# Kernel optimization log

Hardware: AMD Instinct MI355X
Metric: run time of the kernel (lower is better)

The kernel has to match this reference:

```python
import jax, jax.numpy as jnp
import numpy as np

EPS = 1e-6

def setup_inputs() -> dict:
    key = jax.random.key(0)
    ks = jax.random.split(key, 8)
    I, S, O = 1024, 512, 1024
    Bsz, T = 4, 2048
    return {
        "u": jax.random.normal(ks[0], (Bsz, T, I), dtype=jnp.float32),
        "dt": jax.random.normal(ks[1], (S,), dtype=jnp.float32),
        "A": jax.random.normal(ks[2], (S,), dtype=jnp.float32),
        "Bmat": jax.random.normal(ks[3], (I, S), dtype=jnp.float32) / np.sqrt(S),
        "C": jax.random.normal(ks[4], (S, O), dtype=jnp.float32) / np.sqrt(S),
        "D": jax.random.normal(ks[5], (O,), dtype=jnp.float32),
        "norm_w": jnp.ones((I,), dtype=jnp.float32),
    }

def _rmsnorm(x, w):
    x32 = x.astype(jnp.float32)
    n = x32 * jax.lax.rsqrt(jnp.mean(x32 * x32, axis=-1, keepdims=True) + EPS)
    return n.astype(x.dtype) * w

def reference(u, dt, A, Bmat, C, D, norm_w):
    u = _rmsnorm(u, norm_w)                      # [B, T, I]
    Bsz, T, _ = u.shape
    dts = jax.nn.sigmoid(dt)                     # [S]
    a = jnp.exp(-dts * jnp.abs(A))               # [S] discretized decay
    t = jnp.arange(T, dtype=jnp.float32)
    h = dts[:, None] * a[:, None] ** t[None, :]  # [S, T] geometric kernel
    u_proj = jnp.einsum('bti,is->bst', u, Bmat)  # [B, S, T]
    # depthwise causal conv: flipped kernel + cross-correlation == convolution
    k = jnp.flip(h, axis=1)[:, None, :]          # [S, 1, T] (OIW)
    x = jax.lax.conv_general_dilated(
        u_proj, k, window_strides=(1,), padding=[(T - 1, T - 1)],
        dimension_numbers=('NCW', 'OIW', 'NCW'),
        feature_group_count=u_proj.shape[1])[:, :, :T]  # [B, S, T]
    x = jnp.transpose(x, (0, 2, 1))              # [B, T, S]
    y = jnp.einsum('bts,so->bto', x, C) + D      # [B, T, O]
    return (y, x[:, -1])
```

## Files before the change

### kernel.cpp

```cpp
#include <hip/hip_runtime.h>
#include <math.h>

#define I_DIM 1024
#define S_DIM 512
#define O_DIM 1024
#define T_DIM 2048
#define B_SZ 4
#define M_ROWS (B_SZ * T_DIM)
#define EPSF 1e-6f

#define CL 64
#define NCH 32

typedef _Float16 f16;
typedef __attribute__((ext_vector_type(8))) _Float16 f16x8;
typedef __attribute__((ext_vector_type(2))) _Float16 f16x2;
typedef __attribute__((ext_vector_type(4))) float f32x4;

__device__ __forceinline__ unsigned short f2h_bits(float f) {
    _Float16 h = (_Float16)f;
    return __builtin_bit_cast(unsigned short, h);
}

__device__ __forceinline__ void load16_lds(const void* g, void* l) {
    __builtin_amdgcn_global_load_lds((const __attribute__((address_space(1))) void*)g,
                                     (__attribute__((address_space(3))) void*)l,
                                     16, 0, 0);
}

__global__ __launch_bounds__(256)
void prep(const float* __restrict__ u, const float* __restrict__ nw,
          unsigned short* __restrict__ u16,
          const float* __restrict__ Bmat, const float* __restrict__ dt,
          unsigned short* __restrict__ Bt16,
          const float* __restrict__ Cmat, unsigned short* __restrict__ Ct16) {
    __shared__ float tile[32][33];
    const int t = threadIdx.x;
    const int bx = blockIdx.x;

    if (bx < M_ROWS) {
        float4 v = ((const float4*)(u + (size_t)bx * I_DIM))[t];
        float ss = v.x * v.x + v.y * v.y + v.z * v.z + v.w * v.w;
        #pragma unroll
        for (int off = 32; off > 0; off >>= 1) ss += __shfl_down(ss, off, 64);
        if ((t & 63) == 0) tile[0][t >> 6] = ss;
        __syncthreads();
        if (t == 0)
            tile[0][0] = rsqrtf((tile[0][0] + tile[0][1] + tile[0][2] + tile[0][3])
                                * (1.0f / I_DIM) + EPSF);
        __syncthreads();
        const float rs = tile[0][0];
        ushort4 o;
        o.x = f2h_bits(v.x * rs);
        o.y = f2h_bits(v.y * rs);
        o.z = f2h_bits(v.z * rs);
        o.w = f2h_bits(v.w * rs);
        ((ushort4*)(u16 + (size_t)bx * I_DIM))[t] = o;
    } else if (bx < M_ROWS + 512) {
        const int tb = bx - M_ROWS;
        const int bs = (tb & 15) * 32;
        const int bi = (tb >> 4) * 32;
        const int tx = t & 31, ty = t >> 5;
        #pragma unroll
        for (int i = ty; i < 32; i += 8)
            tile[i][tx] = Bmat[(size_t)(bi + i) * S_DIM + bs + tx];
        __syncthreads();
        const float w = nw[bi + tx];
        #pragma unroll
        for (int i = ty; i < 32; i += 8) {
            const int s = bs + i;
            const float dts = 1.0f / (1.0f + expf(-dt[s]));
            Bt16[(size_t)s * I_DIM + bi + tx] = f2h_bits(tile[tx][i] * dts * w);
        }
    } else {
        const int tb = bx - M_ROWS - 512;
        const int bo = (tb & 31) * 32;
        const int bs = (tb >> 5) * 32;
        const int tx = t & 31, ty = t >> 5;
        #pragma unroll
        for (int i = ty; i < 32; i += 8)
            tile[i][tx] = Cmat[(size_t)(bs + i) * O_DIM + bo + tx];
        __syncthreads();
        #pragma unroll
        for (int i = ty; i < 32; i += 8)
            Ct16[(size_t)(bo + i) * S_DIM + bs + tx] = f2h_bits(tile[tx][i]);
    }
}

__global__ __launch_bounds__(256)
void gemm1_chfin(const f16* __restrict__ A, const f16* __restrict__ Bt,
                 f16* __restrict__ up, float* __restrict__ chlast,
                 const float* __restrict__ dt, const float* __restrict__ Avec) {
    constexpr int K = I_DIM, N = S_DIM, NK = K / 32;
    __shared__ f16 As[3][64 * 32];
    __shared__ f16 Bs[3][128 * 32];
    const int t = threadIdx.x;

    int bid = blockIdx.x;
    bid = (bid & 7) * 64 + (bid >> 3);
    const int n0 = (bid & 3) * 128;
    const int m0 = (bid >> 2) * 64;
    const int wid = t >> 6, lane = t & 63;
    const int wn = wid * 32, lr = lane & 15, kg = lane >> 4;

    const int srcswz = ((t & 3) ^ ((t >> 3) & 3)) * 8;
    const f16* aptr = A + (size_t)(m0 + (t >> 2)) * K + srcswz;
    const f16* bptr = Bt + (size_t)(n0 + (t >> 2)) * K + srcswz;
    const int rchunk = (kg ^ ((lr >> 1) & 3)) * 8;

    f32x4 acc[4][2];
    #pragma unroll
    for (int i = 0; i < 4; ++i)
        #pragma unroll
        for (int j = 0; j < 2; ++j) acc[i][j] = (f32x4){0.f, 0.f, 0.f, 0.f};

    auto stage = [&](int kt, int buf) {
        const int k0 = kt * 32;
        load16_lds(aptr + k0, &As[buf][t * 8]);
        load16_lds(bptr + k0, &Bs[buf][t * 8]);
        load16_lds(bptr + (size_t)64 * K + k0, &Bs[buf][2048 + t * 8]);
    };

    stage(0, 0);
    stage(1, 1);
    int bcur = 0, bst = 2;
    for (int kt = 0; kt < NK; ++kt) {
        if (kt + 1 < NK) asm volatile("s_waitcnt vmcnt(3)");
        else             asm volatile("s_waitcnt vmcnt(0)");
        __builtin_amdgcn_s_barrier();
        __builtin_amdgcn_sched_barrier(0);
        if (kt + 2 < NK) stage(kt + 2, bst);

        f16x8 af[4], bf[2];
        #pragma unroll
        for (int m = 0; m < 4; ++m)
            af[m] = *(const f16x8*)&As[bcur][(m * 16 + lr) * 32 + rchunk];
        #pragma unroll
        for (int n = 0; n < 2; ++n)
            bf[n] = *(const f16x8*)&Bs[bcur][(wn + n * 16 + lr) * 32 + rchunk];
        #pragma unroll
        for (int m = 0; m < 4; ++m)
            #pragma unroll
            for (int n = 0; n < 2; ++n)
                acc[m][n] = __builtin_amdgcn_mfma_f32_16x16x32_f16(af[m], bf[n], acc[m][n], 0, 0, 0);

        bcur = (bcur == 2) ? 0 : bcur + 1;
        bst  = (bst  == 2) ? 0 : bst  + 1;
    }

    const int cb = m0 >> 11;
    const int cc = (m0 >> 6) & (NCH - 1);
    #pragma unroll
    for (int n = 0; n < 2; ++n) {
        const int col = n0 + wn + n * 16 + lr;
        const float dts = 1.0f / (1.0f + expf(-dt[col]));
        const float e = dts * fabsf(Avec[col]);
        const float ainv = expf(e);
        float partial = 0.f;
        #pragma unroll
        for (int m = 0; m < 4; ++m) {
            const int row = m * 16 + kg * 4;
            float wgt = expf(-e * (float)(63 - row));
            #pragma unroll
            for (int j = 0; j < 4; ++j) {
                const float val = acc[m][n][j];
                up[(size_t)(m0 + row + j) * N + col] = (_Float16)val;
                partial = fmaf(wgt, val, partial);
                wgt *= ainv;
            }
        }
        partial += __shfl_xor(partial, 16, 64);
        partial += __shfl_xor(partial, 32, 64);
        if (kg == 0)
            chlast[(size_t)(cb * NCH + cc) * S_DIM + col] = partial;
    }
}

__global__ __launch_bounds__(256)
void gemm2_scan(const f16* __restrict__ upb, const float* __restrict__ chlast,
                const f16* __restrict__ Ct, const float* __restrict__ Dvec,
                const float* __restrict__ dt, const float* __restrict__ Avec,
                float* __restrict__ y, float* __restrict__ xlast) {
    constexpr int K = S_DIM, N = O_DIM, NK = K / 32;
    __shared__ __align__(16) unsigned char As[64 * 1024];
    __shared__ f16 Bs[2][128 * 32];
    const int t = threadIdx.x;

    int bid = blockIdx.x;
    bid = (bid & 7) * 128 + (bid >> 3);
    const int n0 = (bid & 7) * 128;
    const int m0 = (bid >> 3) * 64;
    const int wid = t >> 6, lane = t & 63;
    const int wn = wid * 32, lr = lane & 15, kg = lane >> 4;

    const int srcswz = ((t & 3) ^ ((t >> 3) & 3)) * 8;
    const f16* bptr = Ct + (size_t)(n0 + (t >> 2)) * K + srcswz;
    load16_lds(bptr, &Bs[0][t * 8]);
    load16_lds(bptr + (size_t)64 * K, &Bs[0][2048 + t * 8]);
    const int rchunk = (kg ^ ((lr >> 1) & 3)) * 8;

    const int cc = (m0 >> 6) & (NCH - 1);
    const int cb = m0 >> 11;
    const int s0 = 2 * t;
    const float dts0 = 1.0f / (1.0f + expf(-dt[s0]));
    const float dts1 = 1.0f / (1.0f + expf(-dt[s0 + 1]));
    const float ab0 = fabsf(Avec[s0]), ab1 = fabsf(Avec[s0 + 1]);
    const float g0 = expf(-dts0 * ab0);
    const float g1 = expf(-dts1 * ab1);
    const float gCL0 = expf(-dts0 * ab0 * (float)CL);
    const float gCL1 = expf(-dts1 * ab1 * (float)CL);
    const float2* ch = (const float2*)chlast;
    float cy0 = 0.f, cy1 = 0.f;
    {
        int j = 0;
        for (; j + 4 <= cc; j += 4) {
            float2 f0 = ch[(size_t)(cb * NCH + j + 0) * 256 + t];
            float2 f1 = ch[(size_t)(cb * NCH + j + 1) * 256 + t];
            float2 f2 = ch[(size_t)(cb * NCH + j + 2) * 256 + t];
            float2 f3 = ch[(size_t)(cb * NCH + j + 3) * 256 + t];
            cy0 = fmaf(gCL0, cy0, f0.x); cy1 = fmaf(gCL1, cy1, f0.y);
            cy0 = fmaf(gCL0, cy0, f1.x); cy1 = fmaf(gCL1, cy1, f1.y);
            cy0 = fmaf(gCL0, cy0, f2.x); cy1 = fmaf(gCL1, cy1, f2.y);
            cy0 = fmaf(gCL0, cy0, f3.x); cy1 = fmaf(gCL1, cy1, f3.y);
        }
        for (; j < cc; ++j) {
            float2 f = ch[(size_t)(cb * NCH + j) * 256 + t];
            cy0 = fmaf(gCL0, cy0, f.x);
            cy1 = fmaf(gCL1, cy1, f.y);
        }
    }

    const unsigned* up32 = (const unsigned*)upb;
    const size_t ub = (size_t)m0 * 256 + t;
    unsigned v[CL];
    #pragma unroll
    for (int j = 0; j < CL; ++j) v[j] = up32[ub + (size_t)j * 256];
    float x0 = cy0, x1 = cy1;
    #pragma unroll
    for (int j = 0; j < CL; ++j) {
        f16x2 h = __builtin_bit_cast(f16x2, v[j]);
        x0 = fmaf(g0, x0, (float)h.x);
        x1 = fmaf(g1, x1, (float)h.y);
        f16x2 o; o.x = (_Float16)x0; o.y = (_Float16)x1;
        v[j] = __builtin_bit_cast(unsigned, o);
    }
    #pragma unroll
    for (int j = 0; j < CL; ++j)
        *(unsigned*)&As[j * 1024 + ((t * 4) ^ ((j & 7) << 4))] = v[j];
    if (cc == NCH - 1)
        ((float2*)xlast)[cb * 256 + t] = make_float2(x0, x1);
    __syncthreads();

    f32x4 acc[4][2];
    #pragma unroll
    for (int i = 0; i < 4; ++i)
        #pragma unroll
        for (int j = 0; j < 2; ++j) acc[i][j] = (f32x4){0.f, 0.f, 0.f, 0.f};

    const int swz = (lr & 7) << 4;
    for (int kt = 0; kt < NK; ++kt) {
        const int cur = kt & 1;
        if (kt + 1 < NK) {
            const int k1 = (kt + 1) * 32;
            load16_lds(bptr + k1, &Bs[cur ^ 1][t * 8]);
            load16_lds(bptr + (size_t)64 * K + k1, &Bs[cur ^ 1][2048 + t * 8]);
            asm volatile("s_waitcnt vmcnt(2)");
        } else {
            asm volatile("s_waitcnt vmcnt(0)");
        }
        __builtin_amdgcn_s_barrier();
        __builtin_amdgcn_sched_barrier(0);

        f16x8 af[4], bf[2];
        #pragma unroll
        for (int m = 0; m < 4; ++m)
            af[m] = *(const f16x8*)&As[(m * 16 + lr) * 1024 + ((kt * 64 + kg * 16) ^ swz)];
        #pragma unroll
        for (int n = 0; n < 2; ++n)
            bf[n] = *(const f16x8*)&Bs[cur][(wn + n * 16 + lr) * 32 + rchunk];
        #pragma unroll
        for (int m = 0; m < 4; ++m)
            #pragma unroll
            for (int n = 0; n < 2; ++n)
                acc[m][n] = __builtin_amdgcn_mfma_f32_16x16x32_f16(af[m], bf[n], acc[m][n], 0, 0, 0);
        __builtin_amdgcn_s_barrier();
    }

    #pragma unroll
    for (int n = 0; n < 2; ++n) {
        const int col = n0 + wn + n * 16 + lr;
        const float dv = Dvec[col];
        #pragma unroll
        for (int m = 0; m < 4; ++m) {
            const int row = m0 + m * 16 + kg * 4;
            #pragma unroll
            for (int j = 0; j < 4; ++j)
                y[(size_t)(row + j) * N + col] = acc[m][n][j] + dv;
        }
    }
}

extern "C" void kernel_launch(void* const* d_in, const int* in_sizes, int n_in,
                              void* d_out, int out_size, void* d_ws, size_t ws_size,
                              hipStream_t stream) {
    const float* u    = (const float*)d_in[0];
    const float* dt   = (const float*)d_in[1];
    const float* Avec = (const float*)d_in[2];
    const float* Bmat = (const float*)d_in[3];
    const float* Cmat = (const float*)d_in[4];
    const float* Dvec = (const float*)d_in[5];
    const float* nw   = (const float*)d_in[6];

    float* y     = (float*)d_out;
    float* xlast = y + (size_t)M_ROWS * O_DIM;

    char* w = (char*)d_ws;
    unsigned short* u16    = (unsigned short*)(w);
    f16*            up16   = (f16*)(w + 16777216);
    unsigned short* Bt16   = (unsigned short*)(w + 25165824);
    unsigned short* Ct16   = (unsigned short*)(w + 26214400);
    float*          chlast = (float*)(w + 27262976);

    prep<<<M_ROWS + 512 + 512, 256, 0, stream>>>(u, nw, u16, Bmat, dt, Bt16, Cmat, Ct16);

    gemm1_chfin<<<512, 256, 0, stream>>>((const f16*)u16, (const f16*)Bt16,
                                         up16, chlast, dt, Avec);

    gemm2_scan<<<1024, 256, 0, stream>>>(up16, chlast, (const f16*)Ct16, Dvec,
                                         dt, Avec, y, xlast);
}
```

Before: 59.77 us.

## Deepen gemm1 LDS pipeline to five stages and hoist gemm2 chunk loads

The first GEMM now keeps five LDS buffers with four K-tiles in flight instead of three buffers with two, using a fully unrolled loop and stage-specific vmcnt waits. In the second kernel, the 64 per-thread loads of the projected chunk are issued before the carry-in scan over chunk summaries, so their latency overlaps that serial loop. Both kernels also raise wave priority around the MFMA block. The deeper pipeline raises LDS use per block, which may lower occupancy in gemm1, and the hoisted loads hold more registers live during the scan.

```diff
diff --git a/kernel.cpp b/kernel.cpp
--- a/kernel.cpp
+++ b/kernel.cpp
@@ -92,8 +92,8 @@
                  f16* __restrict__ up, float* __restrict__ chlast,
                  const float* __restrict__ dt, const float* __restrict__ Avec) {
     constexpr int K = I_DIM, N = S_DIM, NK = K / 32;
-    __shared__ f16 As[3][64 * 32];
-    __shared__ f16 Bs[3][128 * 32];
+    __shared__ f16 As[5][64 * 32];
+    __shared__ f16 Bs[5][128 * 32];
     const int t = threadIdx.x;
 
     int bid = blockIdx.x;
@@ -103,9 +103,9 @@
     const int wid = t >> 6, lane = t & 63;
     const int wn = wid * 32, lr = lane & 15, kg = lane >> 4;
 
-    const int srcswz = ((t & 3) ^ ((t >> 3) & 3)) * 8;
-    const f16* aptr = A + (size_t)(m0 + (t >> 2)) * K + srcswz;
-    const f16* bptr = Bt + (size_t)(n0 + (t >> 2)) * K + srcswz;
+    const int swch = (t & 3) ^ ((t >> 3) & 3);
+    const f16* aptr = A + (size_t)(m0 + (t >> 2)) * K + swch * 8;
+    const f16* bptr = Bt + (size_t)(n0 + (t >> 2)) * K + swch * 8;
     const int rchunk = (kg ^ ((lr >> 1) & 3)) * 8;
 
     f32x4 acc[4][2];
@@ -114,38 +114,39 @@
         #pragma unroll
         for (int j = 0; j < 2; ++j) acc[i][j] = (f32x4){0.f, 0.f, 0.f, 0.f};
 
-    auto stage = [&](int kt, int buf) {
-        const int k0 = kt * 32;
-        load16_lds(aptr + k0, &As[buf][t * 8]);
-        load16_lds(bptr + k0, &Bs[buf][t * 8]);
-        load16_lds(bptr + (size_t)64 * K + k0, &Bs[buf][2048 + t * 8]);
+    auto stage = [&](int kt, int slot) {
+        load16_lds(aptr + kt * 32, &As[slot][t * 8]);
+        load16_lds(bptr + kt * 32, &Bs[slot][t * 8]);
+        load16_lds(bptr + (size_t)64 * K + kt * 32, &Bs[slot][2048 + t * 8]);
     };
 
-    stage(0, 0);
-    stage(1, 1);
-    int bcur = 0, bst = 2;
+    stage(0, 0); stage(1, 1); stage(2, 2); stage(3, 3);
+
+    #pragma unroll
     for (int kt = 0; kt < NK; ++kt) {
-        if (kt + 1 < NK) asm volatile("s_waitcnt vmcnt(3)");
-        else             asm volatile("s_waitcnt vmcnt(0)");
+        if (kt < NK - 3)       asm volatile("s_waitcnt vmcnt(9)");
+        else if (kt == NK - 3) asm volatile("s_waitcnt vmcnt(6)");
+        else if (kt == NK - 2) asm volatile("s_waitcnt vmcnt(3)");
+        else                   asm volatile("s_waitcnt vmcnt(0)");
         __builtin_amdgcn_s_barrier();
         __builtin_amdgcn_sched_barrier(0);
-        if (kt + 2 < NK) stage(kt + 2, bst);
-
+        if (kt + 4 < NK) stage(kt + 4, (kt + 4) % 5);
+
+        const int slot = kt % 5;
         f16x8 af[4], bf[2];
         #pragma unroll
         for (int m = 0; m < 4; ++m)
-            af[m] = *(const f16x8*)&As[bcur][(m * 16 + lr) * 32 + rchunk];
+            af[m] = *(const f16x8*)&As[slot][(m * 16 + lr) * 32 + rchunk];
         #pragma unroll
         for (int n = 0; n < 2; ++n)
-            bf[n] = *(const f16x8*)&Bs[bcur][(wn + n * 16 + lr) * 32 + rchunk];
+            bf[n] = *(const f16x8*)&Bs[slot][(wn + n * 16 + lr) * 32 + rchunk];
+        __builtin_amdgcn_s_setprio(1);
         #pragma unroll
         for (int m = 0; m < 4; ++m)
             #pragma unroll
             for (int n = 0; n < 2; ++n)
                 acc[m][n] = __builtin_amdgcn_mfma_f32_16x16x32_f16(af[m], bf[n], acc[m][n], 0, 0, 0);
-
-        bcur = (bcur == 2) ? 0 : bcur + 1;
-        bst  = (bst  == 2) ? 0 : bst  + 1;
+        __builtin_amdgcn_s_setprio(0);
     }
 
     const int cb = m0 >> 11;
@@ -195,9 +196,18 @@
 
     const int srcswz = ((t & 3) ^ ((t >> 3) & 3)) * 8;
     const f16* bptr = Ct + (size_t)(n0 + (t >> 2)) * K + srcswz;
-    load16_lds(bptr, &Bs[0][t * 8]);
-    load16_lds(bptr + (size_t)64 * K, &Bs[0][2048 + t * 8]);
+    auto stageB = [&](int kt, int slot) {
+        load16_lds(bptr + kt * 32, &Bs[slot][t * 8]);
+        load16_lds(bptr + (size_t)64 * K + kt * 32, &Bs[slot][2048 + t * 8]);
+    };
+    stageB(0, 0);
     const int rchunk = (kg ^ ((lr >> 1) & 3)) * 8;
+
+    const unsigned* up32 = (const unsigned*)upb;
+    const size_t ub = (size_t)m0 * 256 + t;
+    unsigned v[CL];
+    #pragma unroll
+    for (int j = 0; j < CL; ++j) v[j] = up32[ub + (size_t)j * 256];
 
     const int cc = (m0 >> 6) & (NCH - 1);
     const int cb = m0 >> 11;
@@ -230,11 +240,6 @@
         }
     }
 
-    const unsigned* up32 = (const unsigned*)upb;
-    const size_t ub = (size_t)m0 * 256 + t;
-    unsigned v[CL];
-    #pragma unroll
-    for (int j = 0; j < CL; ++j) v[j] = up32[ub + (size_t)j * 256];
     float x0 = cy0, x1 = cy1;
     #pragma unroll
     for (int j = 0; j < CL; ++j) {
@@ -261,9 +266,7 @@
     for (int kt = 0; kt < NK; ++kt) {
         const int cur = kt & 1;
         if (kt + 1 < NK) {
-            const int k1 = (kt + 1) * 32;
-            load16_lds(bptr + k1, &Bs[cur ^ 1][t * 8]);
-            load16_lds(bptr + (size_t)64 * K + k1, &Bs[cur ^ 1][2048 + t * 8]);
+            stageB(kt + 1, cur ^ 1);
             asm volatile("s_waitcnt vmcnt(2)");
         } else {
             asm volatile("s_waitcnt vmcnt(0)");
@@ -278,11 +281,13 @@
         #pragma unroll
         for (int n = 0; n < 2; ++n)
             bf[n] = *(const f16x8*)&Bs[cur][(wn + n * 16 + lr) * 32 + rchunk];
+        __builtin_amdgcn_s_setprio(1);
         #pragma unroll
         for (int m = 0; m < 4; ++m)
             #pragma unroll
             for (int n = 0; n < 2; ++n)
                 acc[m][n] = __builtin_amdgcn_mfma_f32_16x16x32_f16(af[m], bf[n], acc[m][n], 0, 0, 0);
+        __builtin_amdgcn_s_setprio(0);
         __builtin_amdgcn_s_barrier();
     }
 
```

After: 59.28 us. No clear change (-0.8%).
